# Kernel optimization log

Hardware: AMD Instinct MI355X
Metric: run time of the kernel (lower is better)

Reference implementation:

```python
import jax, jax.numpy as jnp
import numpy as np

EPS_BN = 1e-5
EPS_NORM = 1e-12


def setup_inputs() -> dict:
    dim, mid, k = 128, 32, 3
    b, h, w = 8, 128, 128
    key = jax.random.key(0)
    ks = jax.random.split(key, 16)
    s = 0.05
    return {
        "x": jax.random.normal(ks[0], (b, dim, h, w), jnp.float32),
        "w_spatial_in": jax.random.normal(ks[1], (dim, dim), jnp.float32) * s,
        "w_dw_spatial": jax.random.normal(ks[2], (dim, 1, k), jnp.float32) * s,
        "w_spatial_out": jax.random.normal(ks[3], (dim, dim), jnp.float32) * s,
        "w_ch_in": jax.random.normal(ks[4], (dim, dim), jnp.float32) * s,
        "w_ch_dw": jax.random.normal(ks[5], (dim, 1, k), jnp.float32) * s,
        "w_ch_out": jax.random.normal(ks[6], (dim, dim), jnp.float32) * s,
        "w_mlp1": jax.random.normal(ks[7], (mid, dim), jnp.float32) * s,
        "b_mlp1": jax.random.normal(ks[8], (mid,), jnp.float32) * s,
        "w_mlp2": jax.random.normal(ks[9], (dim, mid), jnp.float32) * s,
        "b_mlp2": jax.random.normal(ks[10], (dim,), jnp.float32) * s,
        "diff_weight": jnp.float32(1.0),
        "bn_gamma": jnp.ones((dim,), jnp.float32),
        "bn_beta": jnp.zeros((dim,), jnp.float32),
        "w_out_proj": jax.random.normal(ks[11], (dim, dim), jnp.float32) * s,
    }


def _dwconv1d(seq, wk):
    # seq: [b, c, L], wk: [c, 1, k] depthwise, 'same' padding
    c = seq.shape[1]
    k = wk.shape[-1]
    return jax.lax.conv_general_dilated(
        seq, wk, window_strides=(1,), padding=[(k // 2, k // 2)],
        dimension_numbers=("NCH", "OIH", "NCH"), feature_group_count=c)


def _ocs_forward(x, w_spatial_in, w_dw_spatial, w_spatial_out,
                 w_ch_in, w_ch_dw, w_ch_out,
                 w_mlp1, b_mlp1, w_mlp2, b_mlp2,
                 diff_weight, bn_gamma, bn_beta, w_out_proj):
    b, c, h, w = x.shape
    L = h * w
    alpha = beta = eta = 1.0

    # ---- scan indices (4 orders) ----
    idx_row = jnp.arange(L)
    gy, gx = jnp.meshgrid(jnp.arange(h), jnp.arange(w), indexing="ij")
    idx_col = (gx * h + gy).reshape(-1)
    orders = [idx_row, idx_row[::-1], idx_col, idx_col[::-1]]

    x_seq0 = x.reshape(b, c, L).transpose(0, 2, 1)  # [b, L, c]

    def scan(idx):
        s = x_seq0[:, idx]                                   # gather   [b,L,c]
        s = jnp.einsum("blc,oc->blo", s, w_spatial_in)       # linear
        s = _dwconv1d(s.transpose(0, 2, 1), w_dw_spatial)    # dw conv  [b,c,L]
        s = jnp.einsum("bcl,oc->blo", s, w_spatial_out)      # linear   [b,L,c]
        s = s.at[:, idx].set(s[:, jnp.arange(L)]) if False else s[:, jnp.argsort(idx)]  # scatter back (inverse perm)
        return s.transpose(0, 2, 1).reshape(b, c, h, w)

    y_sp = (scan(orders[0]) + scan(orders[1]) + scan(orders[2]) + scan(orders[3])) * 0.25

    # ---- channel branch ----
    seq = x.reshape(b, c, L)
    seq = jnp.einsum("oc,bcl->bol", w_ch_in, seq)
    seq = _dwconv1d(seq, w_ch_dw)
    seq = jnp.einsum("oc,bcl->bol", w_ch_out, seq)
    gap = x.mean((2, 3))                                     # [b,c]
    gap = gap / jnp.maximum(jnp.linalg.norm(gap, axis=1, keepdims=True), EPS_NORM)
    m = jnp.einsum("bi,bj->bij", gap, gap)                   # [b,c,c]
    seq_agg = jnp.einsum("bij,bjl->bil", m, seq)             # [b,c,L]
    h1 = jax.nn.silu(jnp.einsum("mc,bcl->bml", w_mlp1, seq_agg) + b_mlp1[None, :, None])
    y_ch = (jnp.einsum("cm,bml->bcl", w_mlp2, h1) + b_mlp2[None, :, None]).reshape(b, c, h, w)

    # ---- difference branch (reflect-pad 4-neighbor abs diff) ----
    p = jnp.pad(x, ((0, 0), (0, 0), (1, 1), (1, 1)), mode="reflect")
    cx = p[:, :, 1:-1, 1:-1]
    diff = (jnp.abs(cx - p[:, :, 1:-1, :-2]) + jnp.abs(cx - p[:, :, 1:-1, 2:])
            + jnp.abs(cx - p[:, :, :-2, 1:-1]) + jnp.abs(cx - p[:, :, 2:, 1:-1])) * 0.25
    y_diff = x + diff_weight * diff

    # ---- combine, 1x1 proj, batchnorm (training-mode batch stats) ----
    y = alpha * y_sp + beta * y_ch + eta * y_diff
    y = jnp.einsum("oc,bchw->bohw", w_out_proj, y)
    mu = y.mean((0, 2, 3))
    var = y.var((0, 2, 3))
    y = (y - mu[None, :, None, None]) * jax.lax.rsqrt(var + EPS_BN)[None, :, None, None]
    y = y * bn_gamma[None, :, None, None] + bn_beta[None, :, None, None]
    return y


def reference(x, w_spatial_in, w_dw_spatial, w_spatial_out, w_ch_in, w_ch_dw,
              w_ch_out, w_mlp1, b_mlp1, w_mlp2, b_mlp2, diff_weight,
              bn_gamma, bn_beta, w_out_proj):
    return _ocs_forward(x, w_spatial_in, w_dw_spatial, w_spatial_out,
                        w_ch_in, w_ch_dw, w_ch_out, w_mlp1, b_mlp1,
                        w_mlp2, b_mlp2, diff_weight, bn_gamma, bn_beta,
                        w_out_proj)
```

## Files before the change

kernel.cpp:

```cpp
#include <hip/hip_runtime.h>
#include <hip/hip_bf16.h>

#define C 128
#define L 16384
#define B 8
#define MID 32
#define NBL (B * L)

typedef unsigned short ushort_t;
typedef __attribute__((ext_vector_type(8))) short s8v;
typedef __attribute__((ext_vector_type(4))) float f4v;

__device__ __forceinline__ unsigned short f2bf(float f) {
    union { float f; unsigned int u; } a; a.f = f;
    unsigned int u = a.u;
    return (unsigned short)((u + 0x7fffu + ((u >> 16) & 1u)) >> 16);
}

__device__ __forceinline__ void load8(const ushort_t* p, float* f) {
    uint4 u = *(const uint4*)p;
    f[0] = __uint_as_float(u.x << 16); f[1] = __uint_as_float(u.x & 0xffff0000u);
    f[2] = __uint_as_float(u.y << 16); f[3] = __uint_as_float(u.y & 0xffff0000u);
    f[4] = __uint_as_float(u.z << 16); f[5] = __uint_as_float(u.z & 0xffff0000u);
    f[6] = __uint_as_float(u.w << 16); f[7] = __uint_as_float(u.w & 0xffff0000u);
}

__device__ __forceinline__ void zero8(float* f) {
#pragma unroll
    for (int j = 0; j < 8; j++) f[j] = 0.f;
}

__device__ __forceinline__ void ld8f(const float* p, float* f) {
    float4 a = *(const float4*)p;
    float4 b = *(const float4*)(p + 4);
    f[0] = a.x; f[1] = a.y; f[2] = a.z; f[3] = a.w;
    f[4] = b.x; f[5] = b.y; f[6] = b.z; f[7] = b.w;
}

__global__ __launch_bounds__(256) void k_cvt(const float* __restrict__ x,
                                             ushort_t* __restrict__ xb,
                                             float* __restrict__ gap) {
    __shared__ float xs[64][129];
    const int bid = blockIdx.x;
    const int b = bid >> 8;
    const int l0 = (bid & 255) * 64;
    const int tid = threadIdx.x;
    const int c = tid >> 1, h = tid & 1;
    const float* src = x + ((size_t)(b * C + c)) * L + l0 + h * 32;
    float s = 0.f;
#pragma unroll
    for (int j = 0; j < 8; j++) {
        float4 v = *(const float4*)(src + j * 4);
        s += (v.x + v.y) + (v.z + v.w);
        int lb = h * 32 + j * 4;
        xs[lb + 0][c] = v.x; xs[lb + 1][c] = v.y;
        xs[lb + 2][c] = v.z; xs[lb + 3][c] = v.w;
    }
    s += __shfl_xor(s, 1);
    if (h == 0) atomicAdd(&gap[b * C + c], s);
    __syncthreads();
    const int l = tid & 63, quarter = tid >> 6, cb = quarter * 32;
    union { ushort_t hh[32]; uint4 q[4]; } u;
#pragma unroll
    for (int k = 0; k < 32; k++) u.hh[k] = f2bf(xs[l][cb + k]);
    uint4* dst = (uint4*)(xb + ((size_t)(b * L + l0 + l)) * C + cb);
#pragma unroll
    for (int k = 0; k < 4; k++) dst[k] = u.q[k];
}

__global__ __launch_bounds__(128) void k_prep_b(const float* __restrict__ gap,
                                                const float* __restrict__ w1,
                                                const float* __restrict__ Wco,
                                                const float* __restrict__ wcd,
                                                float* __restrict__ a,
                                                float* __restrict__ gd0,
                                                float* __restrict__ gd1,
                                                float* __restrict__ gd2) {
    int b = blockIdx.x, c = threadIdx.x;
    __shared__ float gl[C];
    __shared__ float red[C];
    float v = gap[b * C + c] * (1.f / (float)L);
    red[c] = v * v;
    __syncthreads();
    for (int w = 64; w > 0; w >>= 1) {
        if (c < w) red[c] += red[c + w];
        __syncthreads();
    }
    float nrm = fmaxf(sqrtf(red[0]), 1e-12f);
    float gc = v / nrm;
    gl[c] = gc;
    __syncthreads();
    if (c < MID) {
        float s = 0.f;
        for (int k = 0; k < C; k++) s = fmaf(w1[c * C + k], gl[k], s);
        a[b * MID + c] = s;
    }
    {
        float s = 0.f;
        for (int k = 0; k < C; k++) s = fmaf(gl[k], Wco[k * C + c], s);
        gd0[b * C + c] = s * wcd[3 * c];
        gd1[b * C + c] = s * wcd[3 * c + 1];
        gd2[b * C + c] = s * wcd[3 * c + 2];
    }
}

__global__ __launch_bounds__(128) void k_prep_w(const float* __restrict__ Win,
                                                const float* __restrict__ Wci,
                                                const float* __restrict__ Wproj,
                                                const float* __restrict__ Wout,
                                                const float* __restrict__ w2,
                                                const float* __restrict__ b2,
                                                const float* __restrict__ wds,
                                                ushort_t* __restrict__ Wio,
                                                ushort_t* __restrict__ Wcat,
                                                float* __restrict__ bp,
                                                float* __restrict__ kwS,
                                                float* __restrict__ kw1) {
    int o = blockIdx.x, c = threadIdx.x;
    __shared__ float pr[C];
    pr[c] = Wproj[o * C + c];
    __syncthreads();
    Wio[o * C + c] = f2bf(Win[o * C + c]);
    Wio[(C + o) * C + c] = f2bf(Wci[o * C + c]);
    float s = 0.f;
    for (int k = 0; k < C; k++) s = fmaf(pr[k], Wout[k * C + c], s);
    Wcat[o * 288 + c] = f2bf(s);
    Wcat[o * 288 + 128 + c] = f2bf(pr[c]);
    if (c < MID) {
        float s2 = 0.f;
        for (int k = 0; k < C; k++) s2 = fmaf(pr[k], w2[k * MID + c], s2);
        Wcat[o * 288 + 256 + c] = f2bf(s2);
    }
    if (c == 0) {
        float s3 = 0.f;
        for (int k = 0; k < C; k++) s3 = fmaf(pr[k], b2[k], s3);
        bp[o] = s3;
    }
    if (o == 0) {
        kwS[c] = 0.25f * (wds[3 * c] + wds[3 * c + 2]);
        kw1[c] = wds[3 * c + 1];
    }
}

__global__ __launch_bounds__(512, 1) void k_gemm1(const ushort_t* __restrict__ xb,
                                                  const ushort_t* __restrict__ Wio,
                                                  ushort_t* __restrict__ tu) {
    __shared__ ushort_t wl[128 * 136];
    const int tid = threadIdx.x;
    const int bid = blockIdx.x;
    const int b = bid >> 8;
    const int ms = (bid >> 7) & 1;
    const int lt = bid & 127;
    {
        int row = tid >> 2, qq = tid & 3;
        const uint4* s4 = (const uint4*)(Wio + (ms * C + row) * C + qq * 32);
        uint4* d4 = (uint4*)(wl + row * 136 + qq * 32);
        d4[0] = s4[0]; d4[1] = s4[1]; d4[2] = s4[2]; d4[3] = s4[3];
    }
    __syncthreads();
    const int wave = tid >> 6, lane = tid & 63;
    const int l0 = lt * 128 + wave * 16;
    const int n = lane & 15, q = lane >> 4;
    const ushort_t* brow = xb + ((size_t)(b * L + l0 + n)) * C + q * 8;
    s8v bfrag[4];
#pragma unroll
    for (int ks = 0; ks < 4; ks++) bfrag[ks] = *(const s8v*)(brow + ks * 32);
    f4v acc[8];
#pragma unroll
    for (int i = 0; i < 8; i++) acc[i] = (f4v){0.f, 0.f, 0.f, 0.f};
#pragma unroll
    for (int ks = 0; ks < 4; ks++) {
#pragma unroll
        for (int mt = 0; mt < 8; mt++) {
            s8v af = *(const s8v*)(wl + (mt * 16 + n) * 136 + ks * 32 + q * 8);
            acc[mt] = __builtin_amdgcn_mfma_f32_16x16x32_bf16(af, bfrag[ks], acc[mt], 0, 0, 0);
        }
    }
    ushort_t* orow = tu + ((size_t)(b * L + l0 + n)) * 256 + ms * C + q * 4;
#pragma unroll
    for (int mt = 0; mt < 8; mt++) {
        union { ushort_t h[4]; uint2 q2; } u;
#pragma unroll
        for (int i = 0; i < 4; i++) u.h[i] = f2bf(acc[mt][i]);
        *(uint2*)(orow + mt * 16) = u.q2;
    }
}

__global__ __launch_bounds__(512, 4) void k_gemm2f(const ushort_t* __restrict__ tu,
                                                   const ushort_t* __restrict__ xb,
                                                   const ushort_t* __restrict__ Wcat,
                                                   const float* __restrict__ kwS,
                                                   const float* __restrict__ kw1,
                                                   const float* __restrict__ gd0,
                                                   const float* __restrict__ gd1,
                                                   const float* __restrict__ gd2,
                                                   const float* __restrict__ a,
                                                   const float* __restrict__ b1,
                                                   const float* __restrict__ pdw,
                                                   const float* __restrict__ bp,
                                                   float* __restrict__ outp,
                                                   float* __restrict__ stats) {
    __shared__ ushort_t wl[128 * 296];
    const int tid = threadIdx.x;
    const int bid = blockIdx.x;
    const int b = bid >> 7;
    const int y = bid & 127;

#pragma unroll
    for (int i = 0; i < 9; i++) {
        int idx = tid + i * 512;
        int row = idx / 36, col = idx - row * 36;
        *(uint4*)(wl + row * 296 + col * 8) = *(const uint4*)(Wcat + row * 288 + col * 8);
    }

    const int wave = tid >> 6, lane = tid & 63;
    const int n = lane & 15, q = lane >> 4;
    const int xg = wave * 16 + n;
    const int l = y * 128 + xg;
    const size_t rb = (size_t)b * L;

    const int rL = (l > 0) ? (l - 1) : -1;
    const int rR = (l < L - 1) ? (l + 1) : -1;
    const int rU = (y > 0) ? (l - 128) : ((xg > 0) ? (16256 + xg - 1) : -1);
    const int rD = (y < 127) ? (l + 128) : ((xg < 127) ? (xg + 1) : -1);
    const int sL = (xg > 0) ? (l - 1) : (l + 1);
    const int sR = (xg < 127) ? (l + 1) : (l - 1);
    const int sU = (y > 0) ? (l - 128) : (l + 128);
    const int sD = (y < 127) ? (l + 128) : (l - 128);

    float s1 = 0.f;
    {
        const ushort_t* pC = tu + (rb + l) * 256 + 128 + q * 32;
        const ushort_t* pL = (rL >= 0) ? (tu + (rb + rL) * 256 + 128 + q * 32) : (const ushort_t*)0;
        const ushort_t* pR = (rR >= 0) ? (tu + (rb + rR) * 256 + 128 + q * 32) : (const ushort_t*)0;
#pragma unroll
        for (int j = 0; j < 4; j++) {
            float uC[8], uL8[8], uR8[8], g0[8], g1[8], g2[8];
            load8(pC + j * 8, uC);
            if (pL) load8(pL + j * 8, uL8); else zero8(uL8);
            if (pR) load8(pR + j * 8, uR8); else zero8(uR8);
            const int cb2 = b * C + q * 32 + j * 8;
            ld8f(gd0 + cb2, g0); ld8f(gd1 + cb2, g1); ld8f(gd2 + cb2, g2);
#pragma unroll
            for (int j2 = 0; j2 < 8; j2++) {
                s1 = fmaf(g0[j2], uL8[j2], s1);
                s1 = fmaf(g1[j2], uC[j2], s1);
                s1 = fmaf(g2[j2], uR8[j2], s1);
            }
        }
    }
    s1 += __shfl_xor(s1, 16);
    s1 += __shfl_xor(s1, 32);

    const float dwt = pdw[0] * 0.25f;

    f4v acc[8];
#pragma unroll
    for (int i = 0; i < 8; i++) acc[i] = (f4v){0.f, 0.f, 0.f, 0.f};

    __syncthreads();

    {
        const ushort_t* ptC = tu + (rb + l) * 256;
        const ushort_t* ptL = (rL >= 0) ? (tu + (rb + rL) * 256) : (const ushort_t*)0;
        const ushort_t* ptR = (rR >= 0) ? (tu + (rb + rR) * 256) : (const ushort_t*)0;
        const ushort_t* ptU = (rU >= 0) ? (tu + (rb + rU) * 256) : (const ushort_t*)0;
        const ushort_t* ptD = (rD >= 0) ? (tu + (rb + rD) * 256) : (const ushort_t*)0;
#pragma unroll
        for (int ks = 0; ks < 4; ks++) {
            const int c0 = ks * 32 + q * 8;
            float tC[8], tLe[8], tRi[8], tUp[8], tDo[8], kS[8], k1[8];
            load8(ptC + c0, tC);
            if (ptL) load8(ptL + c0, tLe); else zero8(tLe);
            if (ptR) load8(ptR + c0, tRi); else zero8(tRi);
            if (ptU) load8(ptU + c0, tUp); else zero8(tUp);
            if (ptD) load8(ptD + c0, tDo); else zero8(tDo);
            ld8f(kwS + c0, kS); ld8f(kw1 + c0, k1);
            union { ushort_t h[8]; s8v v; } bf;
#pragma unroll
            for (int j = 0; j < 8; j++) {
                float ct = kS[j] * ((tLe[j] + tRi[j]) + (tUp[j] + tDo[j])) + k1[j] * tC[j];
                bf.h[j] = f2bf(ct);
            }
#pragma unroll
            for (int mt = 0; mt < 8; mt++) {
                s8v af = *(const s8v*)(wl + (mt * 16 + n) * 296 + ks * 32 + q * 8);
                acc[mt] = __builtin_amdgcn_mfma_f32_16x16x32_bf16(af, bf.v, acc[mt], 0, 0, 0);
            }
        }
    }

    {
        const ushort_t* pxC = xb + (rb + l) * C;
        const ushort_t* pxL = xb + (rb + sL) * C;
        const ushort_t* pxR = xb + (rb + sR) * C;
        const ushort_t* pxU = xb + (rb + sU) * C;
        const ushort_t* pxD = xb + (rb + sD) * C;
#pragma unroll
        for (int ks = 0; ks < 4; ks++) {
            const int c0 = ks * 32 + q * 8;
            float xC[8], xL8[8], xR8[8], xU8[8], xD8[8];
            load8(pxC + c0, xC);
            load8(pxL + c0, xL8);
            load8(pxR + c0, xR8);
            load8(pxU + c0, xU8);
            load8(pxD + c0, xD8);
            union { ushort_t h[8]; s8v v; } bf;
#pragma unroll
            for (int j = 0; j < 8; j++) {
                float cen = xC[j];
                float d = fabsf(cen - xL8[j]) + fabsf(cen - xR8[j]) +
                          fabsf(cen - xU8[j]) + fabsf(cen - xD8[j]);
                bf.h[j] = f2bf(fmaf(dwt, d, cen));
            }
#pragma unroll
            for (int mt = 0; mt < 8; mt++) {
                s8v af = *(const s8v*)(wl + (mt * 16 + n) * 296 + (4 + ks) * 32 + q * 8);
                acc[mt] = __builtin_amdgcn_mfma_f32_16x16x32_bf16(af, bf.v, acc[mt], 0, 0, 0);
            }
        }
    }

    {
        float av[8], bv[8];
        ld8f(a + b * MID + q * 8, av);
        ld8f(b1 + q * 8, bv);
        union { ushort_t h[8]; s8v v; } bf;
#pragma unroll
        for (int j = 0; j < 8; j++) {
            float pre = fmaf(av[j], s1, bv[j]);
            bf.h[j] = f2bf(pre / (1.f + __expf(-pre)));
        }
#pragma unroll
        for (int mt = 0; mt < 8; mt++) {
            s8v af = *(const s8v*)(wl + (mt * 16 + n) * 296 + 256 + q * 8);
            acc[mt] = __builtin_amdgcn_mfma_f32_16x16x32_bf16(af, bf.v, acc[mt], 0, 0, 0);
        }
    }

#pragma unroll
    for (int mt = 0; mt < 8; mt++) {
        const int o0 = mt * 16 + q * 4;
        float4 bv4 = *(const float4*)(bp + o0);
        float ba[4] = {bv4.x, bv4.y, bv4.z, bv4.w};
#pragma unroll
        for (int i = 0; i < 4; i++) {
            outp[((size_t)(b * C + o0 + i)) * L + l] = acc[mt][i] + ba[i];
        }
    }

    __syncthreads();
    {
        const int o = tid >> 2, seg = tid & 3;
        const float* pr = outp + ((size_t)(b * C + o)) * L + y * 128 + seg * 32;
        float s = 0.f, sq = 0.f;
#pragma unroll
        for (int i = 0; i < 8; i++) {
            float4 v = *(const float4*)(pr + i * 4);
            s += (v.x + v.y) + (v.z + v.w);
            sq += v.x * v.x + v.y * v.y + v.z * v.z + v.w * v.w;
        }
        s += __shfl_xor(s, 1); sq += __shfl_xor(sq, 1);
        s += __shfl_xor(s, 2); sq += __shfl_xor(sq, 2);
        if (seg == 0) {
            atomicAdd(&stats[o], s);
            atomicAdd(&stats[C + o], sq);
        }
    }
}

__global__ void k_bnfin(const float* __restrict__ stats, const float* __restrict__ gamma,
                        const float* __restrict__ beta, float* __restrict__ scsh) {
    int o = threadIdx.x;
    float n = (float)NBL;
    float mu = stats[o] / n;
    float var = stats[C + o] / n - mu * mu;
    float sc = gamma[o] * rsqrtf(var + 1e-5f);
    scsh[o] = sc;
    scsh[C + o] = fmaf(-mu, sc, beta[o]);
}

__global__ __launch_bounds__(256) void k_bnapply(float* __restrict__ outp,
                                                 const float* __restrict__ scsh) {
    int bo = blockIdx.x;
    int o = bo & (C - 1);
    float sc = scsh[o], sh = scsh[C + o];
    float4* p = (float4*)(outp + (size_t)bo * L);
    for (int i = threadIdx.x; i < L / 4; i += 256) {
        float4 v = p[i];
        v.x = fmaf(v.x, sc, sh);
        v.y = fmaf(v.y, sc, sh);
        v.z = fmaf(v.z, sc, sh);
        v.w = fmaf(v.w, sc, sh);
        p[i] = v;
    }
}

extern "C" void kernel_launch(void* const* d_in, const int* in_sizes, int n_in,
                              void* d_out, int out_size, void* d_ws, size_t ws_size,
                              hipStream_t stream) {
    const float* x = (const float*)d_in[0];
    const float* Win = (const float*)d_in[1];
    const float* wds = (const float*)d_in[2];
    const float* Wout = (const float*)d_in[3];
    const float* Wci = (const float*)d_in[4];
    const float* wcd = (const float*)d_in[5];
    const float* Wco = (const float*)d_in[6];
    const float* w1 = (const float*)d_in[7];
    const float* b1 = (const float*)d_in[8];
    const float* w2 = (const float*)d_in[9];
    const float* b2 = (const float*)d_in[10];
    const float* pdw = (const float*)d_in[11];
    const float* gamma = (const float*)d_in[12];
    const float* beta = (const float*)d_in[13];
    const float* Wproj = (const float*)d_in[14];

    char* wsb = (char*)d_ws;
    ushort_t* xb = (ushort_t*)wsb;
    ushort_t* tu = (ushort_t*)(wsb + 33554432);
    float* gd0 = (float*)(wsb + 100663296);
    float* gd1 = (float*)(wsb + 100663296 + 4096);
    float* gd2 = (float*)(wsb + 100663296 + 8192);
    char* S = wsb + 176160768;
    float* gap  = (float*)(S + 0);
    float* stats= (float*)(S + 4096);
    float* scsh = (float*)(S + 5120);
    float* a    = (float*)(S + 6144);
    float* bp   = (float*)(S + 11264);
    float* kwS  = (float*)(S + 11776);
    float* kw1  = (float*)(S + 12288);
    ushort_t* Wio  = (ushort_t*)(S + 14336);
    ushort_t* Wcat = (ushort_t*)(S + 79872);
    float* outp = (float*)d_out;

    hipMemsetAsync(S, 0, 5120, stream);
    k_cvt<<<2048, 256, 0, stream>>>(x, xb, gap);
    k_prep_b<<<8, 128, 0, stream>>>(gap, w1, Wco, wcd, a, gd0, gd1, gd2);
    k_prep_w<<<128, 128, 0, stream>>>(Win, Wci, Wproj, Wout, w2, b2, wds,
                                      Wio, Wcat, bp, kwS, kw1);
    k_gemm1<<<2048, 512, 0, stream>>>(xb, Wio, tu);
    k_gemm2f<<<1024, 512, 0, stream>>>(tu, xb, Wcat, kwS, kw1, gd0, gd1, gd2,
                                       a, b1, pdw, bp, outp, stats);
    k_bnfin<<<1, 128, 0, stream>>>(stats, gamma, beta, scsh);
    k_bnapply<<<1024, 256, 0, stream>>>(outp, scsh);
}
```

Baseline: 344.2 us.

## Fold input projections into output weights and fuse both GEMMs into one kernel

Precomposes the spatial/channel input projections with the depthwise and output weights so the intermediate tu tensor (B*L*256 bf16) no longer needs to be written and re-read. A single fused kernel runs MFMA directly on x and its four neighbours with pre-swizzled LDS weight fragments, and the channel-branch dot product is folded into a per-batch vector. Batch-norm statistics move from the GEMM epilogue into a separate reduction pass over the output. This trades about 2.5x more MFMA work and an extra output read for removing a full GEMM pass and its intermediate memory traffic.

```diff
diff --git a/kernel.cpp b/kernel.cpp
--- a/kernel.cpp
+++ b/kernel.cpp
@@ -17,17 +17,20 @@
     return (unsigned short)((u + 0x7fffu + ((u >> 16) & 1u)) >> 16);
 }
 
-__device__ __forceinline__ void load8(const ushort_t* p, float* f) {
-    uint4 u = *(const uint4*)p;
-    f[0] = __uint_as_float(u.x << 16); f[1] = __uint_as_float(u.x & 0xffff0000u);
-    f[2] = __uint_as_float(u.y << 16); f[3] = __uint_as_float(u.y & 0xffff0000u);
-    f[4] = __uint_as_float(u.z << 16); f[5] = __uint_as_float(u.z & 0xffff0000u);
-    f[6] = __uint_as_float(u.w << 16); f[7] = __uint_as_float(u.w & 0xffff0000u);
-}
-
-__device__ __forceinline__ void zero8(float* f) {
-#pragma unroll
-    for (int j = 0; j < 8; j++) f[j] = 0.f;
+__device__ __forceinline__ float bf2f(short h) {
+    return __uint_as_float(((unsigned int)(unsigned short)h) << 16);
+}
+
+__device__ __forceinline__ void unpack8(s8v v, float* f) {
+#pragma unroll
+    for (int j = 0; j < 8; j++) f[j] = bf2f(v[j]);
+}
+
+__device__ __forceinline__ s8v pack8(const float* f) {
+    s8v v;
+#pragma unroll
+    for (int j = 0; j < 8; j++) v[j] = (short)f2bf(f[j]);
+    return v;
 }
 
 __device__ __forceinline__ void ld8f(const float* p, float* f) {
@@ -35,6 +38,10 @@
     float4 b = *(const float4*)(p + 4);
     f[0] = a.x; f[1] = a.y; f[2] = a.z; f[3] = a.w;
     f[4] = b.x; f[5] = b.y; f[6] = b.z; f[7] = b.w;
+}
+
+__device__ __forceinline__ int widx(int slot, int o, int w) {
+    return ((slot * 8 + (o >> 4)) * 64 + (w >> 3) * 16 + (o & 15)) * 8 + (w & 7);
 }
 
 __global__ __launch_bounds__(256) void k_cvt(const float* __restrict__ x,
@@ -72,13 +79,13 @@
                                                 const float* __restrict__ w1,
                                                 const float* __restrict__ Wco,
                                                 const float* __restrict__ wcd,
+                                                const float* __restrict__ Wci,
                                                 float* __restrict__ a,
-                                                float* __restrict__ gd0,
-                                                float* __restrict__ gd1,
-                                                float* __restrict__ gd2) {
+                                                float* __restrict__ pv) {
     int b = blockIdx.x, c = threadIdx.x;
     __shared__ float gl[C];
     __shared__ float red[C];
+    __shared__ float gws[C];
     float v = gap[b * C + c] * (1.f / (float)L);
     red[c] = v * v;
     __syncthreads();
@@ -87,8 +94,7 @@
         __syncthreads();
     }
     float nrm = fmaxf(sqrtf(red[0]), 1e-12f);
-    float gc = v / nrm;
-    gl[c] = gc;
+    gl[c] = v / nrm;
     __syncthreads();
     if (c < MID) {
         float s = 0.f;
@@ -98,124 +104,89 @@
     {
         float s = 0.f;
         for (int k = 0; k < C; k++) s = fmaf(gl[k], Wco[k * C + c], s);
-        gd0[b * C + c] = s * wcd[3 * c];
-        gd1[b * C + c] = s * wcd[3 * c + 1];
-        gd2[b * C + c] = s * wcd[3 * c + 2];
-    }
+        gws[c] = s;
+    }
+    __syncthreads();
+    float p0 = 0.f, p1 = 0.f, p2 = 0.f;
+    for (int cc = 0; cc < C; cc++) {
+        float wv = Wci[cc * C + c];
+        float g = gws[cc];
+        p0 = fmaf(g * wcd[3 * cc], wv, p0);
+        p1 = fmaf(g * wcd[3 * cc + 1], wv, p1);
+        p2 = fmaf(g * wcd[3 * cc + 2], wv, p2);
+    }
+    pv[b * 384 + c] = p0;
+    pv[b * 384 + 128 + c] = p1;
+    pv[b * 384 + 256 + c] = p2;
 }
 
 __global__ __launch_bounds__(128) void k_prep_w(const float* __restrict__ Win,
-                                                const float* __restrict__ Wci,
                                                 const float* __restrict__ Wproj,
                                                 const float* __restrict__ Wout,
                                                 const float* __restrict__ w2,
                                                 const float* __restrict__ b2,
                                                 const float* __restrict__ wds,
-                                                ushort_t* __restrict__ Wio,
-                                                ushort_t* __restrict__ Wcat,
-                                                float* __restrict__ bp,
-                                                float* __restrict__ kwS,
-                                                float* __restrict__ kw1) {
+                                                ushort_t* __restrict__ Wf,
+                                                float* __restrict__ bp) {
     int o = blockIdx.x, c = threadIdx.x;
     __shared__ float pr[C];
+    __shared__ float wct[C];
     pr[c] = Wproj[o * C + c];
     __syncthreads();
-    Wio[o * C + c] = f2bf(Win[o * C + c]);
-    Wio[(C + o) * C + c] = f2bf(Wci[o * C + c]);
-    float s = 0.f;
-    for (int k = 0; k < C; k++) s = fmaf(pr[k], Wout[k * C + c], s);
-    Wcat[o * 288 + c] = f2bf(s);
-    Wcat[o * 288 + 128 + c] = f2bf(pr[c]);
+    {
+        float s = 0.f;
+        for (int k = 0; k < C; k++) s = fmaf(pr[k], Wout[k * C + c], s);
+        wct[c] = s;
+    }
+    __syncthreads();
+    float a1 = 0.f, as = 0.f;
+    for (int cc = 0; cc < C; cc++) {
+        float w = wct[cc];
+        float win = Win[cc * C + c];
+        a1 = fmaf(w * wds[3 * cc + 1], win, a1);
+        as = fmaf(w * (0.25f * (wds[3 * cc] + wds[3 * cc + 2])), win, as);
+    }
+    const int slot = c >> 5, wi = c & 31;
+    Wf[widx(slot, o, wi)] = f2bf(a1);
+    Wf[widx(4 + slot, o, wi)] = f2bf(as);
+    Wf[widx(8 + slot, o, wi)] = f2bf(pr[c]);
     if (c < MID) {
         float s2 = 0.f;
         for (int k = 0; k < C; k++) s2 = fmaf(pr[k], w2[k * MID + c], s2);
-        Wcat[o * 288 + 256 + c] = f2bf(s2);
+        Wf[widx(12, o, c)] = f2bf(s2);
     }
     if (c == 0) {
         float s3 = 0.f;
         for (int k = 0; k < C; k++) s3 = fmaf(pr[k], b2[k], s3);
         bp[o] = s3;
     }
-    if (o == 0) {
-        kwS[c] = 0.25f * (wds[3 * c] + wds[3 * c + 2]);
-        kw1[c] = wds[3 * c + 1];
-    }
-}
-
-__global__ __launch_bounds__(512, 1) void k_gemm1(const ushort_t* __restrict__ xb,
-                                                  const ushort_t* __restrict__ Wio,
-                                                  ushort_t* __restrict__ tu) {
-    __shared__ ushort_t wl[128 * 136];
-    const int tid = threadIdx.x;
-    const int bid = blockIdx.x;
-    const int b = bid >> 8;
-    const int ms = (bid >> 7) & 1;
-    const int lt = bid & 127;
-    {
-        int row = tid >> 2, qq = tid & 3;
-        const uint4* s4 = (const uint4*)(Wio + (ms * C + row) * C + qq * 32);
-        uint4* d4 = (uint4*)(wl + row * 136 + qq * 32);
-        d4[0] = s4[0]; d4[1] = s4[1]; d4[2] = s4[2]; d4[3] = s4[3];
-    }
-    __syncthreads();
-    const int wave = tid >> 6, lane = tid & 63;
-    const int l0 = lt * 128 + wave * 16;
-    const int n = lane & 15, q = lane >> 4;
-    const ushort_t* brow = xb + ((size_t)(b * L + l0 + n)) * C + q * 8;
-    s8v bfrag[4];
-#pragma unroll
-    for (int ks = 0; ks < 4; ks++) bfrag[ks] = *(const s8v*)(brow + ks * 32);
-    f4v acc[8];
-#pragma unroll
-    for (int i = 0; i < 8; i++) acc[i] = (f4v){0.f, 0.f, 0.f, 0.f};
-#pragma unroll
-    for (int ks = 0; ks < 4; ks++) {
-#pragma unroll
-        for (int mt = 0; mt < 8; mt++) {
-            s8v af = *(const s8v*)(wl + (mt * 16 + n) * 136 + ks * 32 + q * 8);
-            acc[mt] = __builtin_amdgcn_mfma_f32_16x16x32_bf16(af, bfrag[ks], acc[mt], 0, 0, 0);
-        }
-    }
-    ushort_t* orow = tu + ((size_t)(b * L + l0 + n)) * 256 + ms * C + q * 4;
-#pragma unroll
-    for (int mt = 0; mt < 8; mt++) {
-        union { ushort_t h[4]; uint2 q2; } u;
-#pragma unroll
-        for (int i = 0; i < 4; i++) u.h[i] = f2bf(acc[mt][i]);
-        *(uint2*)(orow + mt * 16) = u.q2;
-    }
-}
-
-__global__ __launch_bounds__(512, 4) void k_gemm2f(const ushort_t* __restrict__ tu,
-                                                   const ushort_t* __restrict__ xb,
-                                                   const ushort_t* __restrict__ Wcat,
-                                                   const float* __restrict__ kwS,
-                                                   const float* __restrict__ kw1,
-                                                   const float* __restrict__ gd0,
-                                                   const float* __restrict__ gd1,
-                                                   const float* __restrict__ gd2,
+}
+
+__global__ __launch_bounds__(1024, 4) void k_fused(const ushort_t* __restrict__ xb,
+                                                   const ushort_t* __restrict__ Wf,
+                                                   const float* __restrict__ pv,
                                                    const float* __restrict__ a,
                                                    const float* __restrict__ b1,
                                                    const float* __restrict__ pdw,
                                                    const float* __restrict__ bp,
-                                                   float* __restrict__ outp,
-                                                   float* __restrict__ stats) {
-    __shared__ ushort_t wl[128 * 296];
+                                                   float* __restrict__ outp) {
+    __shared__ ushort_t wlf[53248];
     const int tid = threadIdx.x;
-    const int bid = blockIdx.x;
-    const int b = bid >> 7;
-    const int y = bid & 127;
-
-#pragma unroll
-    for (int i = 0; i < 9; i++) {
-        int idx = tid + i * 512;
-        int row = idx / 36, col = idx - row * 36;
-        *(uint4*)(wl + row * 296 + col * 8) = *(const uint4*)(Wcat + row * 288 + col * 8);
+    int bid = blockIdx.x;
+    bid = (bid & 7) * 64 + (bid >> 3);
+    const int b = bid >> 6;
+    const int y0 = (bid & 63) << 1;
+
+#pragma unroll
+    for (int i = 0; i < 7; i++) {
+        int idx = tid + i * 1024;
+        if (idx < 6656) ((uint4*)wlf)[idx] = ((const uint4*)Wf)[idx];
     }
 
     const int wave = tid >> 6, lane = tid & 63;
     const int n = lane & 15, q = lane >> 4;
-    const int xg = wave * 16 + n;
+    const int y = y0 + (wave >> 3);
+    const int xg = (wave & 7) * 16 + n;
     const int l = y * 128 + xg;
     const size_t rb = (size_t)b * L;
 
@@ -228,115 +199,117 @@
     const int sU = (y > 0) ? (l - 128) : (l + 128);
     const int sD = (y < 127) ? (l + 128) : (l - 128);
 
+    const float dwt4 = pdw[0] * 0.25f;
+    const ushort_t* xrow = xb + (rb + l) * C;
+
+    s8v fxc[4], fyd[4];
     float s1 = 0.f;
-    {
-        const ushort_t* pC = tu + (rb + l) * 256 + 128 + q * 32;
-        const ushort_t* pL = (rL >= 0) ? (tu + (rb + rL) * 256 + 128 + q * 32) : (const ushort_t*)0;
-        const ushort_t* pR = (rR >= 0) ? (tu + (rb + rR) * 256 + 128 + q * 32) : (const ushort_t*)0;
-#pragma unroll
-        for (int j = 0; j < 4; j++) {
-            float uC[8], uL8[8], uR8[8], g0[8], g1[8], g2[8];
-            load8(pC + j * 8, uC);
-            if (pL) load8(pL + j * 8, uL8); else zero8(uL8);
-            if (pR) load8(pR + j * 8, uR8); else zero8(uR8);
-            const int cb2 = b * C + q * 32 + j * 8;
-            ld8f(gd0 + cb2, g0); ld8f(gd1 + cb2, g1); ld8f(gd2 + cb2, g2);
-#pragma unroll
-            for (int j2 = 0; j2 < 8; j2++) {
-                s1 = fmaf(g0[j2], uL8[j2], s1);
-                s1 = fmaf(g1[j2], uC[j2], s1);
-                s1 = fmaf(g2[j2], uR8[j2], s1);
-            }
+#pragma unroll
+    for (int ks = 0; ks < 4; ks++) {
+        const int c0 = ks * 32 + q * 8;
+        s8v vc = *(const s8v*)(xrow + c0);
+        fxc[ks] = vc;
+        float xc[8]; unpack8(vc, xc);
+        float xsl[8], xsr[8], xsu[8], xsd[8];
+        unpack8(*(const s8v*)(xb + (rb + sL) * C + c0), xsl);
+        unpack8(*(const s8v*)(xb + (rb + sR) * C + c0), xsr);
+        unpack8(*(const s8v*)(xb + (rb + sU) * C + c0), xsu);
+        unpack8(*(const s8v*)(xb + (rb + sD) * C + c0), xsd);
+        float yd8[8];
+#pragma unroll
+        for (int j = 0; j < 8; j++) {
+            float d = fabsf(xc[j] - xsl[j]) + fabsf(xc[j] - xsr[j]) +
+                      fabsf(xc[j] - xsu[j]) + fabsf(xc[j] - xsd[j]);
+            yd8[j] = fmaf(dwt4, d, xc[j]);
+        }
+        fyd[ks] = pack8(yd8);
+
+        const int rlc = (rL >= 0) ? rL : 0;
+        const int rrc = (rR >= 0) ? rR : 0;
+        float xl1[8], xr1[8];
+        unpack8(*(const s8v*)(xb + (rb + rlc) * C + c0), xl1);
+        unpack8(*(const s8v*)(xb + (rb + rrc) * C + c0), xr1);
+        if (rL < 0) {
+#pragma unroll
+            for (int j = 0; j < 8; j++) xl1[j] = 0.f;
+        }
+        if (rR < 0) {
+#pragma unroll
+            for (int j = 0; j < 8; j++) xr1[j] = 0.f;
+        }
+        float p0v[8], p1v[8], p2v[8];
+        ld8f(pv + b * 384 + c0, p0v);
+        ld8f(pv + b * 384 + 128 + c0, p1v);
+        ld8f(pv + b * 384 + 256 + c0, p2v);
+#pragma unroll
+        for (int j = 0; j < 8; j++) {
+            s1 = fmaf(p1v[j], xc[j], s1);
+            s1 = fmaf(p0v[j], xl1[j], s1);
+            s1 = fmaf(p2v[j], xr1[j], s1);
         }
     }
     s1 += __shfl_xor(s1, 16);
     s1 += __shfl_xor(s1, 32);
 
-    const float dwt = pdw[0] * 0.25f;
-
-    f4v acc[8];
-#pragma unroll
-    for (int i = 0; i < 8; i++) acc[i] = (f4v){0.f, 0.f, 0.f, 0.f};
-
-    __syncthreads();
-
-    {
-        const ushort_t* ptC = tu + (rb + l) * 256;
-        const ushort_t* ptL = (rL >= 0) ? (tu + (rb + rL) * 256) : (const ushort_t*)0;
-        const ushort_t* ptR = (rR >= 0) ? (tu + (rb + rR) * 256) : (const ushort_t*)0;
-        const ushort_t* ptU = (rU >= 0) ? (tu + (rb + rU) * 256) : (const ushort_t*)0;
-        const ushort_t* ptD = (rD >= 0) ? (tu + (rb + rD) * 256) : (const ushort_t*)0;
-#pragma unroll
-        for (int ks = 0; ks < 4; ks++) {
-            const int c0 = ks * 32 + q * 8;
-            float tC[8], tLe[8], tRi[8], tUp[8], tDo[8], kS[8], k1[8];
-            load8(ptC + c0, tC);
-            if (ptL) load8(ptL + c0, tLe); else zero8(tLe);
-            if (ptR) load8(ptR + c0, tRi); else zero8(tRi);
-            if (ptU) load8(ptU + c0, tUp); else zero8(tUp);
-            if (ptD) load8(ptD + c0, tDo); else zero8(tDo);
-            ld8f(kwS + c0, kS); ld8f(kw1 + c0, k1);
-            union { ushort_t h[8]; s8v v; } bf;
-#pragma unroll
-            for (int j = 0; j < 8; j++) {
-                float ct = kS[j] * ((tLe[j] + tRi[j]) + (tUp[j] + tDo[j])) + k1[j] * tC[j];
-                bf.h[j] = f2bf(ct);
-            }
-#pragma unroll
-            for (int mt = 0; mt < 8; mt++) {
-                s8v af = *(const s8v*)(wl + (mt * 16 + n) * 296 + ks * 32 + q * 8);
-                acc[mt] = __builtin_amdgcn_mfma_f32_16x16x32_bf16(af, bf.v, acc[mt], 0, 0, 0);
-            }
-        }
-    }
-
-    {
-        const ushort_t* pxC = xb + (rb + l) * C;
-        const ushort_t* pxL = xb + (rb + sL) * C;
-        const ushort_t* pxR = xb + (rb + sR) * C;
-        const ushort_t* pxU = xb + (rb + sU) * C;
-        const ushort_t* pxD = xb + (rb + sD) * C;
-#pragma unroll
-        for (int ks = 0; ks < 4; ks++) {
-            const int c0 = ks * 32 + q * 8;
-            float xC[8], xL8[8], xR8[8], xU8[8], xD8[8];
-            load8(pxC + c0, xC);
-            load8(pxL + c0, xL8);
-            load8(pxR + c0, xR8);
-            load8(pxU + c0, xU8);
-            load8(pxD + c0, xD8);
-            union { ushort_t h[8]; s8v v; } bf;
-#pragma unroll
-            for (int j = 0; j < 8; j++) {
-                float cen = xC[j];
-                float d = fabsf(cen - xL8[j]) + fabsf(cen - xR8[j]) +
-                          fabsf(cen - xU8[j]) + fabsf(cen - xD8[j]);
-                bf.h[j] = f2bf(fmaf(dwt, d, cen));
-            }
-#pragma unroll
-            for (int mt = 0; mt < 8; mt++) {
-                s8v af = *(const s8v*)(wl + (mt * 16 + n) * 296 + (4 + ks) * 32 + q * 8);
-                acc[mt] = __builtin_amdgcn_mfma_f32_16x16x32_bf16(af, bf.v, acc[mt], 0, 0, 0);
-            }
-        }
-    }
-
+    s8v fs;
     {
         float av[8], bv[8];
         ld8f(a + b * MID + q * 8, av);
         ld8f(b1 + q * 8, bv);
-        union { ushort_t h[8]; s8v v; } bf;
 #pragma unroll
         for (int j = 0; j < 8; j++) {
             float pre = fmaf(av[j], s1, bv[j]);
-            bf.h[j] = f2bf(pre / (1.f + __expf(-pre)));
-        }
-#pragma unroll
-        for (int mt = 0; mt < 8; mt++) {
-            s8v af = *(const s8v*)(wl + (mt * 16 + n) * 296 + 256 + q * 8);
-            acc[mt] = __builtin_amdgcn_mfma_f32_16x16x32_bf16(af, bf.v, acc[mt], 0, 0, 0);
-        }
-    }
+            fs[j] = (short)f2bf(pre / (1.f + __expf(-pre)));
+        }
+    }
+
+    f4v acc[8];
+#pragma unroll
+    for (int i = 0; i < 8; i++) acc[i] = (f4v){0.f, 0.f, 0.f, 0.f};
+
+    __syncthreads();
+
+#define AF(slot, mt) (*(const s8v*)(wlf + ((((slot) * 8 + (mt)) * 64 + lane) * 8)))
+
+#pragma unroll
+    for (int ks = 0; ks < 4; ks++)
+#pragma unroll
+        for (int mt = 0; mt < 8; mt++)
+            acc[mt] = __builtin_amdgcn_mfma_f32_16x16x32_bf16(AF(ks, mt), fxc[ks], acc[mt], 0, 0, 0);
+
+    const int nbr[4] = {rL, rR, rU, rD};
+#pragma unroll
+    for (int t = 0; t < 4; t++) {
+        const int r = nbr[t];
+        const int rc = (r >= 0) ? r : 0;
+        s8v fn[4];
+#pragma unroll
+        for (int ks = 0; ks < 4; ks++) {
+            s8v v = *(const s8v*)(xb + (rb + rc) * C + ks * 32 + q * 8);
+            if (r < 0) {
+#pragma unroll
+                for (int j = 0; j < 8; j++) v[j] = 0;
+            }
+            fn[ks] = v;
+        }
+#pragma unroll
+        for (int ks = 0; ks < 4; ks++)
+#pragma unroll
+            for (int mt = 0; mt < 8; mt++)
+                acc[mt] = __builtin_amdgcn_mfma_f32_16x16x32_bf16(AF(4 + ks, mt), fn[ks], acc[mt], 0, 0, 0);
+    }
+
+#pragma unroll
+    for (int ks = 0; ks < 4; ks++)
+#pragma unroll
+        for (int mt = 0; mt < 8; mt++)
+            acc[mt] = __builtin_amdgcn_mfma_f32_16x16x32_bf16(AF(8 + ks, mt), fyd[ks], acc[mt], 0, 0, 0);
+
+#pragma unroll
+    for (int mt = 0; mt < 8; mt++)
+        acc[mt] = __builtin_amdgcn_mfma_f32_16x16x32_bf16(AF(12, mt), fs, acc[mt], 0, 0, 0);
+
+#undef AF
 
 #pragma unroll
     for (int mt = 0; mt < 8; mt++) {
@@ -348,24 +321,32 @@
             outp[((size_t)(b * C + o0 + i)) * L + l] = acc[mt][i] + ba[i];
         }
     }
-
-    __syncthreads();
-    {
-        const int o = tid >> 2, seg = tid & 3;
-        const float* pr = outp + ((size_t)(b * C + o)) * L + y * 128 + seg * 32;
-        float s = 0.f, sq = 0.f;
-#pragma unroll
-        for (int i = 0; i < 8; i++) {
-            float4 v = *(const float4*)(pr + i * 4);
-            s += (v.x + v.y) + (v.z + v.w);
-            sq += v.x * v.x + v.y * v.y + v.z * v.z + v.w * v.w;
-        }
-        s += __shfl_xor(s, 1); sq += __shfl_xor(sq, 1);
-        s += __shfl_xor(s, 2); sq += __shfl_xor(sq, 2);
-        if (seg == 0) {
-            atomicAdd(&stats[o], s);
-            atomicAdd(&stats[C + o], sq);
-        }
+}
+
+__global__ __launch_bounds__(256) void k_bnstats2(const float* __restrict__ outp,
+                                                  float* __restrict__ stats) {
+    const int bo = blockIdx.x;
+    const int o = bo & (C - 1);
+    const float4* p = (const float4*)(outp + (size_t)bo * L);
+    float s = 0.f, sq = 0.f;
+    for (int i = threadIdx.x; i < L / 4; i += 256) {
+        float4 v = p[i];
+        s += (v.x + v.y) + (v.z + v.w);
+        sq += v.x * v.x + v.y * v.y + v.z * v.z + v.w * v.w;
+    }
+    __shared__ float rs[256], rq[256];
+    rs[threadIdx.x] = s; rq[threadIdx.x] = sq;
+    __syncthreads();
+    for (int w = 128; w > 0; w >>= 1) {
+        if (threadIdx.x < w) {
+            rs[threadIdx.x] += rs[threadIdx.x + w];
+            rq[threadIdx.x] += rq[threadIdx.x + w];
+        }
+        __syncthreads();
+    }
+    if (threadIdx.x == 0) {
+        atomicAdd(&stats[o], rs[0]);
+        atomicAdd(&stats[C + o], rq[0]);
     }
 }
 
@@ -417,30 +398,22 @@
 
     char* wsb = (char*)d_ws;
     ushort_t* xb = (ushort_t*)wsb;
-    ushort_t* tu = (ushort_t*)(wsb + 33554432);
-    float* gd0 = (float*)(wsb + 100663296);
-    float* gd1 = (float*)(wsb + 100663296 + 4096);
-    float* gd2 = (float*)(wsb + 100663296 + 8192);
+    ushort_t* Wf = (ushort_t*)(wsb + 33554432);
     char* S = wsb + 176160768;
     float* gap  = (float*)(S + 0);
     float* stats= (float*)(S + 4096);
     float* scsh = (float*)(S + 5120);
     float* a    = (float*)(S + 6144);
-    float* bp   = (float*)(S + 11264);
-    float* kwS  = (float*)(S + 11776);
-    float* kw1  = (float*)(S + 12288);
-    ushort_t* Wio  = (ushort_t*)(S + 14336);
-    ushort_t* Wcat = (ushort_t*)(S + 79872);
+    float* bp   = (float*)(S + 8192);
+    float* pv   = (float*)(S + 12288);
     float* outp = (float*)d_out;
 
     hipMemsetAsync(S, 0, 5120, stream);
     k_cvt<<<2048, 256, 0, stream>>>(x, xb, gap);
-    k_prep_b<<<8, 128, 0, stream>>>(gap, w1, Wco, wcd, a, gd0, gd1, gd2);
-    k_prep_w<<<128, 128, 0, stream>>>(Win, Wci, Wproj, Wout, w2, b2, wds,
-                                      Wio, Wcat, bp, kwS, kw1);
-    k_gemm1<<<2048, 512, 0, stream>>>(xb, Wio, tu);
-    k_gemm2f<<<1024, 512, 0, stream>>>(tu, xb, Wcat, kwS, kw1, gd0, gd1, gd2,
-                                       a, b1, pdw, bp, outp, stats);
+    k_prep_b<<<8, 128, 0, stream>>>(gap, w1, Wco, wcd, Wci, a, pv);
+    k_prep_w<<<128, 128, 0, stream>>>(Win, Wproj, Wout, w2, b2, wds, Wf, bp);
+    k_fused<<<512, 1024, 0, stream>>>(xb, Wf, pv, a, b1, pdw, bp, outp);
+    k_bnstats2<<<1024, 256, 0, stream>>>(outp, stats);
     k_bnfin<<<1, 128, 0, stream>>>(stats, gamma, beta, scsh);
     k_bnapply<<<1024, 256, 0, stream>>>(outp, scsh);
 }
```

Measured after the change: 643.1 us. 1.87x slower.
